# Performance work log

Measured on AMD Instinct MI355X. Metric: run time of the kernel, lower is better.

Reference implementation:

```python
import jax, jax.numpy as jnp
import numpy as np


def _min_euclid_block(x, sh):
    # x: [B, C, T], sh: [C, K, S]
    S = sh.shape[-1]
    T = x.shape[2]
    W = T - S + 1  # number of sliding windows
    idx = jnp.arange(W)[:, None] + jnp.arange(S)[None, :]  # [W, S]
    xu = x[:, :, idx]  # [B, C, W, S] sliding windows (unfold)
    # pairwise euclidean distance via the Gram expansion (same math as cdist)
    x2 = jnp.sum(xu * xu, axis=-1)          # [B, C, W]
    s2 = jnp.sum(sh * sh, axis=-1)          # [C, K]
    xs = jnp.einsum('bcws,cks->bcwk', xu, sh)  # [B, C, W, K]
    d2 = x2[..., None] + s2[None, :, None, :] - 2.0 * xs
    d = jnp.sqrt(jnp.maximum(d2, 1e-12))    # [B, C, W, K]
    d = jnp.sum(d, axis=1, keepdims=True)   # sum over channels -> [B, 1, W, K]
    return jnp.min(d, axis=2)               # min over windows -> [B, 1, K]


def setup_inputs() -> dict:
    key = jax.random.key(0)
    k0, k1, k2, k3 = jax.random.split(key, 4)
    B, C, T, K = 32, 3, 2048, 128
    return {
        'x': jax.random.normal(k0, (B, C, T), dtype=jnp.float32),
        'sh16': jax.random.normal(k1, (C, K, 16), dtype=jnp.float32),
        'sh32': jax.random.normal(k2, (C, K, 32), dtype=jnp.float32),
        'sh64': jax.random.normal(k3, (C, K, 64), dtype=jnp.float32),
    }


def reference(x, sh16, sh32, sh64):
    # ShapeletsDistBlocks with dist_measure='euclidean': run each
    # MinEuclideanDistBlock and concatenate along the shapelet axis (dim 2).
    outs = [_min_euclid_block(x, sh) for sh in (sh16, sh32, sh64)]
    return jnp.concatenate(outs, axis=2)  # [B, 1, sum(K)]
```

## Files before the change

### kernel.cpp

```cpp
#include <hip/hip_runtime.h>

typedef __attribute__((ext_vector_type(8)))  __bf16 bf16x8;
typedef __attribute__((ext_vector_type(16))) float  f32x16;

#define DEV __device__ __forceinline__

namespace {

constexpr int BB = 32, CC = 3, TT = 2048, KK = 128, OUTK = 384;
constexpr int TP = 2176;

constexpr size_t OFF_B16 = 0;
constexpr size_t OFF_B32 = 12288;
constexpr size_t OFF_B64 = 36864;
constexpr size_t OFF_S2  = 86016;
constexpr size_t OFF_X2  = 90624;
constexpr size_t OFF_XC  = 2449920;

DEV unsigned short rne(float f) {
  unsigned u = __float_as_uint(f);
  u += 0x7FFFu + ((u >> 16) & 1u);
  return (unsigned short)(u >> 16);
}
DEV float rnef(float f) {
  unsigned u = __float_as_uint(f);
  u += 0x7FFFu + ((u >> 16) & 1u);
  return __uint_as_float(u & 0xFFFF0000u);
}
DEV uint4 pack8(const unsigned short* h) {
  uint4 d;
  d.x = (unsigned)h[0] | ((unsigned)h[1] << 16);
  d.y = (unsigned)h[2] | ((unsigned)h[3] << 16);
  d.z = (unsigned)h[4] | ((unsigned)h[5] << 16);
  d.w = (unsigned)h[6] | ((unsigned)h[7] << 16);
  return d;
}
DEV float f4get(const float4 v, int j) {
  switch (j) { case 0: return v.x; case 1: return v.y; case 2: return v.z; default: return v.w; }
}

constexpr int N_OUT = BB * OUTK;
constexpr int N_BF  = 5376;
constexpr int N_S2  = 1152;
constexpr int N_XC  = BB * CC * 8 * (TP/8);
constexpr int N_X2  = BB * CC * TT;
constexpr int N_TOT = N_OUT + N_BF + N_S2 + N_XC + N_X2;

__global__ __launch_bounds__(256) void precompute(
    const float* __restrict__ x, const float* __restrict__ sh16,
    const float* __restrict__ sh32, const float* __restrict__ sh64,
    unsigned char* __restrict__ ws, unsigned* __restrict__ outu)
{
  int i = blockIdx.x * 256 + threadIdx.x;
  if (i >= N_TOT) return;
  if (i < N_OUT) { outu[i] = 0x7f800000u; return; }
  i -= N_OUT;

  if (i < N_BF) {
    int S, it; const float* sh; size_t boff;
    if (i < 768)       { S = 16; it = i;        sh = sh16; boff = OFF_B16; }
    else if (i < 2304) { S = 32; it = i - 768;  sh = sh32; boff = OFF_B32; }
    else               { S = 64; it = i - 2304; sh = sh64; boff = OFF_B64; }
    const int CHS = S / 8, KST = S / 16;
    int c = it / (KK * CHS); int r = it - c * KK * CHS;
    int n = r / CHS;         int k0 = (r - n * CHS) * 8;
    const float* src = sh + ((size_t)(c * KK + n)) * S + k0;
    unsigned short h[8];
    #pragma unroll
    for (int j = 0; j < 8; ++j) h[j] = rne(src[j]);
    ((uint4*)(ws + boff))[((c * 4 + (n >> 5)) * KST + (k0 >> 4)) * 64 + ((k0 >> 3) & 1) * 32 + (n & 31)] = pack8(h);
    return;
  }
  i -= N_BF;

  if (i < N_S2) {
    int Sidx = i / 384; int r = i - Sidx * 384; int c = r >> 7; int k = r & 127;
    int S = 16 << Sidx;
    const float* sh = (Sidx == 0) ? sh16 : ((Sidx == 1) ? sh32 : sh64);
    const float* sp = sh + ((size_t)(c * KK + k)) * S;
    float acc = 0.f;
    #pragma unroll 4
    for (int s = 0; s < S; ++s) { float v = rnef(sp[s]); acc = fmaf(v, v, acc); }
    ((float*)(ws + OFF_S2))[(Sidx * CC + c) * KK + k] = acc;
    return;
  }
  i -= N_S2;

  if (i < N_XC) {
    const int per = TP / 8;
    int c8 = i / per; int q8 = i - c8 * per;
    int p  = c8 & 7;  int bc = c8 >> 3;
    const float* xb = x + (size_t)bc * TT;
    int m0 = q8 * 8;
    unsigned short h[8];
    #pragma unroll
    for (int j = 0; j < 8; ++j) {
      int mi = m0 + j + p;
      float v = (mi < TT) ? xb[mi] : 0.f;
      h[j] = rne(v);
    }
    ((uint4*)(ws + OFF_XC + (size_t)c8 * TP * 2))[q8] = pack8(h);
    return;
  }
  i -= N_XC;

  {
    int w = i & (TT - 1); int bc = i >> 11;
    const float* xb = x + (size_t)bc * TT;
    float acc = 0.f, a16, a32, a64;
    #pragma unroll 4
    for (int s = 0; s < 16; ++s) { int mi = w + s; float v = (mi < TT) ? rnef(xb[mi]) : 0.f; acc = fmaf(v, v, acc); }
    a16 = acc;
    #pragma unroll 4
    for (int s = 16; s < 32; ++s) { int mi = w + s; float v = (mi < TT) ? rnef(xb[mi]) : 0.f; acc = fmaf(v, v, acc); }
    a32 = acc;
    #pragma unroll 4
    for (int s = 32; s < 64; ++s) { int mi = w + s; float v = (mi < TT) ? rnef(xb[mi]) : 0.f; acc = fmaf(v, v, acc); }
    a64 = acc;
    float* x2 = (float*)(ws + OFF_X2);
    x2[(size_t)(0 * BB * CC + bc) * TT + w] = a16;
    x2[(size_t)(1 * BB * CC + bc) * TT + w] = a32;
    x2[(size_t)(2 * BB * CC + bc) * TT + w] = a64;
  }
}

DEV void epi(const f32x16 a, const float* __restrict__ x2c, float s2c, int lhi, f32x16& dsum) {
  #pragma unroll
  for (int g = 0; g < 4; ++g) {
    const float4 xq = *(const float4*)(x2c + 4 * lhi + 8 * g);
    #pragma unroll
    for (int j = 0; j < 4; ++j) {
      const int r2 = g * 4 + j;
      dsum[r2] += __builtin_amdgcn_sqrtf(fmaxf(fmaf(-2.f, a[r2], f4get(xq, j) + s2c), 1e-12f));
    }
  }
}

template<int S, int KST, int OUTOFF, size_t BOFF, int SIDX>
DEV void run(const unsigned char* __restrict__ ws, unsigned* __restrict__ outu,
             int r, float* __restrict__ x2l, float* __restrict__ s2l)
{
  const int b = r >> 4, wg = r & 15;
  const int tid = (int)threadIdx.x;
  const int lane = tid & 63, wsub = tid >> 6;
  const int l31 = lane & 31, lhi = lane >> 5, p = l31 & 7;
  const int w0 = wg * 128 + wsub * 32;

  const float* x2g = (const float*)(ws + OFF_X2) + (size_t)(SIDX * BB * CC + b * CC) * TT + wg * 128;
  const float* s2g = (const float*)(ws + OFF_S2) + SIDX * CC * KK;
  #pragma unroll
  for (int i0 = 0; i0 < 2; ++i0) {
    int i = i0 * 256 + tid;
    if (i < 384) {
      int c = i >> 7, q = i & 127;
      x2l[i] = x2g[(size_t)c * TT + q];
      s2l[i] = s2g[c * KK + q];
    }
  }
  __syncthreads();

  const unsigned short* XCb = (const unsigned short*)(ws + OFF_XC);
  uint4 A[CC][KST];
  #pragma unroll
  for (int c = 0; c < CC; ++c) {
    const unsigned short* xA = XCb + ((size_t)((b * CC + c) * 8) + p) * TP
                             + (w0 + 8 * (l31 >> 3) + 8 * lhi);
    #pragma unroll
    for (int kk = 0; kk < KST; ++kk) A[c][kk] = *(const uint4*)(xA + 16 * kk);
  }

  const uint4* Bg = (const uint4*)(ws + BOFF) + lane;
  constexpr int W = TT - S + 1;

  #pragma unroll
  for (int kq = 0; kq < 4; ++kq) {
    f32x16 dsum{};
    #pragma unroll
    for (int c = 0; c < CC; ++c) {
      uint4 Bf[KST];
      #pragma unroll
      for (int kk = 0; kk < KST; ++kk)
        Bf[kk] = Bg[(size_t)(((c * 4 + kq) * KST + kk)) * 64];
      f32x16 acc{};
      #pragma unroll
      for (int kk = 0; kk < KST; ++kk)
        acc = __builtin_amdgcn_mfma_f32_32x32x16_bf16(
            __builtin_bit_cast(bf16x8, A[c][kk]), __builtin_bit_cast(bf16x8, Bf[kk]), acc, 0, 0, 0);
      const float s2c = s2l[c * 128 + kq * 32 + l31];
      epi(acc, x2l + c * 128 + wsub * 32, s2c, lhi, dsum);
    }
    float m = __builtin_inff();
    if (w0 + 31 < W) {
      #pragma unroll
      for (int r2 = 0; r2 < 16; ++r2) m = fminf(m, dsum[r2]);
    } else {
      #pragma unroll
      for (int r2 = 0; r2 < 16; ++r2) {
        const int ro = (r2 & 3) + 8 * (r2 >> 2) + 4 * lhi;
        if (w0 + ro < W) m = fminf(m, dsum[r2]);
      }
    }
    m = fminf(m, __shfl_xor(m, 32));
    if (lane < 32)
      atomicMin(outu + (b * OUTK + OUTOFF + kq * 32 + l31), __float_as_uint(m));
  }
}

__global__ __launch_bounds__(256, 3) void shapelets_main(
    const unsigned char* __restrict__ ws, unsigned* __restrict__ outu)
{
  __shared__ __attribute__((aligned(16))) float x2l[384];
  __shared__ __attribute__((aligned(16))) float s2l[384];
  const int j    = (int)blockIdx.x;
  const int bl   = j & 7;
  const int midx = j >> 3;
  const int wg   = midx & 15;
  const int bh   = (midx >> 4) & 3;
  const int So   = midx >> 6;
  const int r    = (bh * 8 + bl) * 16 + wg;
  if (So == 0)      run<64, 4, 256, OFF_B64, 2>(ws, outu, r, x2l, s2l);
  else if (So == 1) run<32, 2, 128, OFF_B32, 1>(ws, outu, r, x2l, s2l);
  else              run<16, 1,   0, OFF_B16, 0>(ws, outu, r, x2l, s2l);
}

}

extern "C" void kernel_launch(void* const* d_in, const int* in_sizes, int n_in,
                              void* d_out, int out_size, void* d_ws, size_t ws_size,
                              hipStream_t stream) {
  const float* x    = (const float*)d_in[0];
  const float* sh16 = (const float*)d_in[1];
  const float* sh32 = (const float*)d_in[2];
  const float* sh64 = (const float*)d_in[3];
  unsigned* outu = (unsigned*)d_out;
  unsigned char* ws = (unsigned char*)d_ws;

  precompute<<<(N_TOT + 255) / 256, 256, 0, stream>>>(x, sh16, sh32, sh64, ws, outu);
  shapelets_main<<<1536, 256, 0, stream>>>(ws, outu);
}
```

Measured before the change: 39.54 us.

## Double-buffer B fragment loads, hoist A loads, and block-reduce mins before atomics

```diff
diff --git a/kernel.cpp b/kernel.cpp
--- a/kernel.cpp
+++ b/kernel.cpp
@@ -138,7 +138,8 @@
 
 template<int S, int KST, int OUTOFF, size_t BOFF, int SIDX>
 DEV void run(const unsigned char* __restrict__ ws, unsigned* __restrict__ outu,
-             int r, float* __restrict__ x2l, float* __restrict__ s2l)
+             int r, float* __restrict__ x2l, float* __restrict__ s2l,
+             float* __restrict__ mred)
 {
   const int b = r >> 4, wg = r & 15;
   const int tid = (int)threadIdx.x;
@@ -146,6 +147,22 @@
   const int l31 = lane & 31, lhi = lane >> 5, p = l31 & 7;
   const int w0 = wg * 128 + wsub * 32;
 
+  const uint4* Bg = (const uint4*)(ws + BOFF) + lane;
+
+  uint4 Bb[2][KST];
+  #pragma unroll
+  for (int kk = 0; kk < KST; ++kk) Bb[0][kk] = Bg[(size_t)kk * 64];
+
+  const unsigned short* XCb = (const unsigned short*)(ws + OFF_XC);
+  uint4 A[CC][KST];
+  #pragma unroll
+  for (int c = 0; c < CC; ++c) {
+    const unsigned short* xA = XCb + ((size_t)((b * CC + c) * 8) + p) * TP
+                             + (w0 + 8 * (l31 >> 3) + 8 * lhi);
+    #pragma unroll
+    for (int kk = 0; kk < KST; ++kk) A[c][kk] = *(const uint4*)(xA + 16 * kk);
+  }
+
   const float* x2g = (const float*)(ws + OFF_X2) + (size_t)(SIDX * BB * CC + b * CC) * TT + wg * 128;
   const float* s2g = (const float*)(ws + OFF_S2) + SIDX * CC * KK;
   #pragma unroll
@@ -159,33 +176,28 @@
   }
   __syncthreads();
 
-  const unsigned short* XCb = (const unsigned short*)(ws + OFF_XC);
-  uint4 A[CC][KST];
-  #pragma unroll
-  for (int c = 0; c < CC; ++c) {
-    const unsigned short* xA = XCb + ((size_t)((b * CC + c) * 8) + p) * TP
-                             + (w0 + 8 * (l31 >> 3) + 8 * lhi);
-    #pragma unroll
-    for (int kk = 0; kk < KST; ++kk) A[c][kk] = *(const uint4*)(xA + 16 * kk);
-  }
-
-  const uint4* Bg = (const uint4*)(ws + BOFF) + lane;
   constexpr int W = TT - S + 1;
+  float mq[4];
 
   #pragma unroll
   for (int kq = 0; kq < 4; ++kq) {
     f32x16 dsum{};
     #pragma unroll
     for (int c = 0; c < CC; ++c) {
-      uint4 Bf[KST];
-      #pragma unroll
-      for (int kk = 0; kk < KST; ++kk)
-        Bf[kk] = Bg[(size_t)(((c * 4 + kq) * KST + kk)) * 64];
+      const int g  = kq * CC + c;
+      const int pb = g & 1;
+      if (g < 4 * CC - 1) {
+        const int ng = g + 1;
+        const int nkq = ng / CC, nc = ng - nkq * CC;
+        #pragma unroll
+        for (int kk = 0; kk < KST; ++kk)
+          Bb[pb ^ 1][kk] = Bg[(size_t)(((nc * 4 + nkq) * KST + kk)) * 64];
+      }
       f32x16 acc{};
       #pragma unroll
       for (int kk = 0; kk < KST; ++kk)
         acc = __builtin_amdgcn_mfma_f32_32x32x16_bf16(
-            __builtin_bit_cast(bf16x8, A[c][kk]), __builtin_bit_cast(bf16x8, Bf[kk]), acc, 0, 0, 0);
+            __builtin_bit_cast(bf16x8, A[c][kk]), __builtin_bit_cast(bf16x8, Bb[pb][kk]), acc, 0, 0, 0);
       const float s2c = s2l[c * 128 + kq * 32 + l31];
       epi(acc, x2l + c * 128 + wsub * 32, s2c, lhi, dsum);
     }
@@ -200,9 +212,19 @@
         if (w0 + ro < W) m = fminf(m, dsum[r2]);
       }
     }
-    m = fminf(m, __shfl_xor(m, 32));
-    if (lane < 32)
-      atomicMin(outu + (b * OUTK + OUTOFF + kq * 32 + l31), __float_as_uint(m));
+    mq[kq] = fminf(m, __shfl_xor(m, 32));
+  }
+
+  if (lane < 32) {
+    #pragma unroll
+    for (int kq = 0; kq < 4; ++kq) mred[(wsub * 4 + kq) * 32 + l31] = mq[kq];
+  }
+  __syncthreads();
+  if (tid < 128) {
+    const int kq = tid >> 5, q = tid & 31;
+    float v = fminf(fminf(mred[(0 * 4 + kq) * 32 + q], mred[(1 * 4 + kq) * 32 + q]),
+                    fminf(mred[(2 * 4 + kq) * 32 + q], mred[(3 * 4 + kq) * 32 + q]));
+    atomicMin(outu + (b * OUTK + OUTOFF + kq * 32 + q), __float_as_uint(v));
   }
 }
 
@@ -211,6 +233,7 @@
 {
   __shared__ __attribute__((aligned(16))) float x2l[384];
   __shared__ __attribute__((aligned(16))) float s2l[384];
+  __shared__ __attribute__((aligned(16))) float mred[512];
   const int j    = (int)blockIdx.x;
   const int bl   = j & 7;
   const int midx = j >> 3;
@@ -218,9 +241,9 @@
   const int bh   = (midx >> 4) & 3;
   const int So   = midx >> 6;
   const int r    = (bh * 8 + bl) * 16 + wg;
-  if (So == 0)      run<64, 4, 256, OFF_B64, 2>(ws, outu, r, x2l, s2l);
-  else if (So == 1) run<32, 2, 128, OFF_B32, 1>(ws, outu, r, x2l, s2l);
-  else              run<16, 1,   0, OFF_B16, 0>(ws, outu, r, x2l, s2l);
+  if (So == 0)      run<64, 4, 256, OFF_B64, 2>(ws, outu, r, x2l, s2l, mred);
+  else if (So == 1) run<32, 2, 128, OFF_B32, 1>(ws, outu, r, x2l, s2l, mred);
+  else              run<16, 1,   0, OFF_B16, 0>(ws, outu, r, x2l, s2l, mred);
 }
 
 }
```

New measurement: 39.40 us, median of 2. About the same (-0.4%).
